# Kernel tuning notes

Hardware: AMD Instinct MI355X
Metric: run time of the kernel (lower is better)

The kernel has to match this reference:

```python
import jax, jax.numpy as jnp
import numpy as np

N = 8192          # points
M = 3             # point dimension
K_ORDER = 4       # tensor order k
C = 64            # input_in_channel
KNN = 16          # n_neighbors
NEG_SLOPE = 0.2
EPS = 1e-6


def vn_leaky_relu(v, U, neg_slope=NEG_SLOPE, eps=EPS):
    """Vector-neuron LeakyReLU. v: (n, T, C), U: (C, C) learned direction map."""
    d = jnp.einsum('ntc,cd->ntd', v, U)
    dot = jnp.sum(v * d, axis=1, keepdims=True)        # (n,1,C)
    dn2 = jnp.sum(d * d, axis=1, keepdims=True)        # (n,1,C)
    proj = (dot / (dn2 + eps)) * d
    return neg_slope * v + (1.0 - neg_slope) * jnp.where(dot >= 0, v, v - proj)


def contract_pairs(x, w, k):
    """Learned combination of all pairwise traces.
    x: (n, m,...,m (k axes), C); w: (k*(k-1)//2, C). Returns order k-2 tensor."""
    pairs = [(a, b) for a in range(1, k + 1) for b in range(a + 1, k + 1)]
    acc = None
    for i, (a, b) in enumerate(pairs):
        t = jnp.trace(x, axis1=a, axis2=b)             # (n, m^(k-2)..., C)
        acc = t * w[i] if acc is None else acc + t * w[i]
    return acc


def setup_inputs() -> dict:
    key = jax.random.key(0)
    ks = jax.random.split(key, 8)
    s1 = 1.0 / np.sqrt(C)
    s2 = 1.0 / np.sqrt(2 * C)
    return {
        'x': jax.random.normal(ks[0], (N, M), dtype=jnp.float32),
        'kron_W': jax.random.normal(ks[1], (K_ORDER, C, C), dtype=jnp.float32) * s1,
        'kron_U': jax.random.normal(ks[2], (K_ORDER, C, C), dtype=jnp.float32) * s1,
        'contr_w4': jax.random.normal(ks[3], (6, 2 * C), dtype=jnp.float32) * s2,
        'contr_W': jax.random.normal(ks[4], (2 * C, 2 * C), dtype=jnp.float32) * s2,
        'contr_U': jax.random.normal(ks[5], (2 * C, 2 * C), dtype=jnp.float32) * s2,
        'contr_w2': jax.random.normal(ks[6], (1, 2 * C), dtype=jnp.float32) * s2,
    }


def reference(x, kron_W, kron_U, contr_w4, contr_W, contr_U, contr_w2):
    n, m = x.shape
    c = kron_W.shape[-1]
    # --- brute-force kNN on x (replaces sklearn fit/kneighbors; self included,
    # static because dynamic_knn=False) ---
    sq = jnp.sum(x * x, axis=1)
    d2 = sq[:, None] + sq[None, :] - 2.0 * (x @ x.T)   # (n,n)
    _, idx = jax.lax.top_k(-d2, KNN)                   # (n,KNN) neighbor indices
    xg = x[idx]                                        # (n,KNN,m) gathered coords
    # --- Kronecker stage: v_{t+1}[i] = mean_{j in N(i)} x_j (x) v_t[j] ---
    v = jnp.ones((n, 1, c), dtype=x.dtype)
    for t in range(kron_W.shape[0]):
        vg = v[idx]                                    # (n,KNN,m^t,c)
        v = jnp.einsum('nka,nkbc->nabc', xg, vg) / KNN # (n,m,m^t,c)
        v = v.reshape(n, -1, c)                        # (n,m^(t+1),c)
        v = v @ kron_W[t]                              # CustomLinear (no bias)
        v = vn_leaky_relu(v, kron_U[t])
    # --- mean pooling + concat (pool_type=mean) ---
    g = jnp.mean(v, axis=0, keepdims=True)
    v = jnp.concatenate([v, jnp.broadcast_to(g, v.shape)], axis=2)  # (n,m^k,2c)
    c2 = 2 * c
    k = kron_W.shape[0]
    h = v.reshape((n,) + (m,) * k + (c2,))             # (n,3,3,3,3,2c)
    # --- contraction stage: k=4 -> 2 -> 0 ---
    h = contract_pairs(h, contr_w4, k)                 # (n,m,m,2c)
    h = h.reshape(n, m * m, c2) @ contr_W              # CustomLinear
    h = vn_leaky_relu(h, contr_U)
    h = h.reshape(n, m, m, c2)
    out = contract_pairs(h, contr_w2, 2)               # (n,2c)
    return out
```

## Files before the change

### kernel.cpp

```cpp
#include <hip/hip_runtime.h>
#include <math.h>

#define NPTS 8192
#define KNB  16
#define C1   64
#define C2   128
#define NEG  0.2f
#define VEPS 1e-6f
#define NCH  32
#define CHSZ (NPTS/NCH)

__device__ __forceinline__ unsigned long long expand10(unsigned v) {
    unsigned long long r = v & 0x3FFu;
    r = (r | (r << 16)) & 0x030000FFULL;
    r = (r | (r <<  8)) & 0x0300F00FULL;
    r = (r | (r <<  4)) & 0x030C30C3ULL;
    r = (r | (r <<  2)) & 0x09249249ULL;
    return r;
}

__global__ __launch_bounds__(256) void keys_kernel(const float* __restrict__ x,
                                                   unsigned long long* __restrict__ keys)
{
    const int i = blockIdx.x * 256 + threadIdx.x;
    auto cell = [](float v) -> unsigned {
        float t = (v + 6.f) * (1024.f / 12.f);
        int c = (int)t;
        c = c < 0 ? 0 : (c > 1023 ? 1023 : c);
        return (unsigned)c;
    };
    const unsigned long long m = expand10(cell(x[3*i+0]))
                               | (expand10(cell(x[3*i+1])) << 1)
                               | (expand10(cell(x[3*i+2])) << 2);
    keys[i] = (m << 13) | (unsigned long long)i;
}

__global__ __launch_bounds__(256) void rank_zero(int* __restrict__ rk)
{
    rk[blockIdx.x * 256 + threadIdx.x] = 0;
}

__global__ __launch_bounds__(256) void rank_part(const unsigned long long* __restrict__ keys,
                                                 int* __restrict__ rk)
{
    __shared__ unsigned long long sk[1024];
    const int slice = blockIdx.x & 7;
    const int qg    = blockIdx.x >> 3;
    for (int j = threadIdx.x; j < 1024; j += 256) sk[j] = keys[slice*1024 + j];
    __syncthreads();
    const int i = qg*256 + threadIdx.x;
    const unsigned long long mine = keys[i];
    int r = 0;
    for (int j = 0; j < 1024; j += 4)
        r += (int)(sk[j] < mine) + (int)(sk[j+1] < mine)
           + (int)(sk[j+2] < mine) + (int)(sk[j+3] < mine);
    atomicAdd(&rk[i], r);
}

__global__ __launch_bounds__(256) void rank_scatter(const int* __restrict__ rk,
                                                    const float* __restrict__ x,
                                                    float* __restrict__ xp,
                                                    int* __restrict__ perm)
{
    const int i = blockIdx.x * 256 + threadIdx.x;
    const int r = rk[i];
    perm[r] = i;
    xp[3*r+0] = x[3*i+0]; xp[3*r+1] = x[3*i+1]; xp[3*r+2] = x[3*i+2];
}

__global__ __launch_bounds__(256) void seedthr_kernel(const float* __restrict__ xp,
                                                      float* __restrict__ gthr)
{
    const int q = blockIdx.x * 256 + threadIdx.x;
    const float qx = xp[3*q+0], qy = xp[3*q+1], qz = xp[3*q+2];
    int lo = q - 7; lo = lo < 0 ? 0 : (lo > NPTS-16 ? NPTS-16 : lo);
    float mx = 0.f;
#pragma unroll
    for (int s = 0; s < 16; ++s) {
        const float dx = qx - xp[3*(lo+s)+0];
        const float dy = qy - xp[3*(lo+s)+1];
        const float dz = qz - xp[3*(lo+s)+2];
        mx = fmaxf(mx, fmaf(dx, dx, fmaf(dy, dy, dz*dz)));
    }
    gthr[q] = mx * 1.0002f;
}

__global__ __launch_bounds__(256) void aabb_kernel(const float* __restrict__ xp,
                                                   float* __restrict__ gaabb)
{
    __shared__ float wred[4][6];
    const int chunk = blockIdx.x;
    const int tid = threadIdx.x;
    const int j = chunk * CHSZ + tid;
    float mnx = xp[3*j+0], mny = xp[3*j+1], mnz = xp[3*j+2];
    float mxx = mnx, mxy = mny, mxz = mnz;
    for (int off = 32; off > 0; off >>= 1) {
        mnx = fminf(mnx, __shfl_down(mnx, off));
        mny = fminf(mny, __shfl_down(mny, off));
        mnz = fminf(mnz, __shfl_down(mnz, off));
        mxx = fmaxf(mxx, __shfl_down(mxx, off));
        mxy = fmaxf(mxy, __shfl_down(mxy, off));
        mxz = fmaxf(mxz, __shfl_down(mxz, off));
    }
    if ((tid & 63) == 0) {
        const int w = tid >> 6;
        wred[w][0]=mnx; wred[w][1]=mny; wred[w][2]=mnz;
        wred[w][3]=mxx; wred[w][4]=mxy; wred[w][5]=mxz;
    }
    __syncthreads();
    if (tid == 0) {
        float a0=wred[0][0], a1=wred[0][1], a2=wred[0][2];
        float a3=wred[0][3], a4=wred[0][4], a5=wred[0][5];
        for (int w = 1; w < 4; ++w) {
            a0=fminf(a0,wred[w][0]); a1=fminf(a1,wred[w][1]); a2=fminf(a2,wred[w][2]);
            a3=fmaxf(a3,wred[w][3]); a4=fmaxf(a4,wred[w][4]); a5=fmaxf(a5,wred[w][5]);
        }
        gaabb[chunk*8+0]=a0; gaabb[chunk*8+1]=a1; gaabb[chunk*8+2]=a2;
        gaabb[chunk*8+3]=a3; gaabb[chunk*8+4]=a4; gaabb[chunk*8+5]=a5;
    }
}

__global__ __launch_bounds__(256) void knn_part(const float* __restrict__ x,
                                                const float* __restrict__ gthr,
                                                const float* __restrict__ gaabb,
                                                unsigned long long* __restrict__ parts)
{
    __shared__ __align__(16) float4 cpt[4 * CHSZ];
    __shared__ unsigned long long sbuf[256 * 9];

    const int tid   = threadIdx.x;
    const int wv    = tid >> 6;
    const int lane  = tid & 63;
    const int chunk = blockIdx.x & (NCH - 1);
    const int qg    = blockIdx.x >> 5;
    const int j0    = chunk * CHSZ;
    const int q     = qg * 256 + tid;

    const float qx = x[3*q+0], qy = x[3*q+1], qz = x[3*q+2];
    float thrF = gthr[q];

    {
        const float dx = fmaxf(0.f, fmaxf(gaabb[chunk*8+0] - qx, qx - gaabb[chunk*8+3]));
        const float dy = fmaxf(0.f, fmaxf(gaabb[chunk*8+1] - qy, qy - gaabb[chunk*8+4]));
        const float dz = fmaxf(0.f, fmaxf(gaabb[chunk*8+2] - qz, qz - gaabb[chunk*8+5]));
        const float lb = fmaf(dx, dx, fmaf(dy, dy, dz*dz)) * 0.9998f;
        if (__all(lb > thrF)) {
#pragma unroll
            for (int r = 0; r < 16; ++r)
                parts[((size_t)chunk * KNB + r) * NPTS + q] = ~0ull;
            return;
        }
    }

    float4* wcpt = cpt + wv * CHSZ;
#pragma unroll
    for (int s = 0; s < 4; ++s) {
        const int j = lane + 64*s;
        wcpt[j] = make_float4(x[3*(j0+j)+0], x[3*(j0+j)+1], x[3*(j0+j)+2], 0.f);
    }

    unsigned long long bd[16];
#pragma unroll
    for (int r = 0; r < 16; ++r) bd[r] = ~0ull;
    int cnt = 0;
    unsigned long long* mybuf = sbuf + tid * 9;

    auto flush = [&]() {
#pragma unroll
        for (int s = 0; s < 8; ++s) {
            if (s < cnt) {
                const unsigned long long k = mybuf[s];
                if (k < bd[15]) {
#pragma unroll
                    for (int p2 = 15; p2 > 0; --p2) {
                        const bool sh = k < bd[p2-1];
                        const bool pl = k < bd[p2];
                        bd[p2] = sh ? bd[p2-1] : (pl ? k : bd[p2]);
                    }
                    if (k < bd[0]) bd[0] = k;
                }
            }
        }
        cnt = 0;
        if (bd[15] != ~0ull) {
            const double dub = __longlong_as_double((long long)(bd[15] | 8191ull));
            thrF = fminf(thrF, (float)dub * 1.0001f);
        }
    };

    for (int jj = 0; jj < CHSZ; jj += 4) {
        const float4 p0 = wcpt[jj+0];
        const float4 p1 = wcpt[jj+1];
        const float4 p2 = wcpt[jj+2];
        const float4 p3 = wcpt[jj+3];
#pragma unroll
        for (int u = 0; u < 4; ++u) {
            const float4 p = (u==0) ? p0 : (u==1) ? p1 : (u==2) ? p2 : p3;
            const float dx = qx - p.x, dy = qy - p.y, dz = qz - p.z;
            const float d2f = fmaf(dx, dx, fmaf(dy, dy, dz*dz));
            if (d2f <= thrF) {
                const double ddx = (double)dx, ddy = (double)dy, ddz = (double)dz;
                const double d2 = ddx*ddx + ddy*ddy + ddz*ddz;
                const unsigned long long key =
                    (((unsigned long long)__double_as_longlong(d2)) & ~8191ull)
                    | (unsigned long long)(j0 + jj + u);
                if (key < bd[15]) { mybuf[cnt] = key; ++cnt; }
            }
        }
        if (__any(cnt >= 5)) flush();
    }
    flush();

#pragma unroll
    for (int r = 0; r < 16; ++r)
        parts[((size_t)chunk * KNB + r) * NPTS + q] = bd[r];
}

__global__ __launch_bounds__(256) void knn_merge(const unsigned long long* __restrict__ parts,
                                                 int* __restrict__ idx_out)
{
    __shared__ unsigned char heads[256][NCH];
    const int tid = threadIdx.x;
    const int q = blockIdx.x * 256 + tid;
    unsigned char* h = heads[tid];
#pragma unroll
    for (int c = 0; c < NCH; ++c) h[c] = 0;
    for (int r = 0; r < KNB; ++r) {
        unsigned long long best = ~0ull; int bc = 0;
#pragma unroll
        for (int c = 0; c < NCH; ++c) {
            const unsigned long long k = parts[((size_t)c * KNB + h[c]) * NPTS + q];
            if (k < best) { best = k; bc = c; }
        }
        h[bc]++;
        idx_out[q*KNB + r] = (int)(best & 8191ull);
    }
}

__global__ __launch_bounds__(256) void prep_kernel(const float* __restrict__ kW,
                                                   const float* __restrict__ kU,
                                                   float* __restrict__ scol,
                                                   float* __restrict__ bcat)
{
    __shared__ float sW[64*64];
    __shared__ float sS[64];
    const int t = blockIdx.x;
    const int tid = threadIdx.x;
    if (t == 0) {
        for (int e = tid; e < 64*64; e += 256) sW[e] = kW[e];
        __syncthreads();
        if (tid < 64) {
            float s = 0.f;
            for (int j = 0; j < 64; ++j) s += sW[j*64 + tid];
            sS[tid] = s;
        }
        __syncthreads();
        if (tid < 64) {
            float s2 = 0.f;
            for (int j = 0; j < 64; ++j) s2 = fmaf(sS[j], kU[j*64 + tid], s2);
            scol[tid]      = sS[tid];
            scol[64 + tid] = s2;
        }
    } else {
        const float* W = kW + t*4096;
        const float* U = kU + t*4096;
        for (int e = tid; e < 64*64; e += 256) sW[e] = W[e];
        __syncthreads();
        float* B = bcat + (size_t)(t-1)*64*128;
        for (int o = tid; o < 64*64; o += 256) {
            const int j = o >> 6, c = o & 63;
            float s = 0.f;
            for (int l = 0; l < 64; ++l) s = fmaf(sW[j*64 + l], U[l*64 + c], s);
            B[j*128 + c]      = sW[j*64 + c];
            B[j*128 + 64 + c] = s;
        }
    }
}

__global__ __launch_bounds__(256) void step1_kernel(const float* __restrict__ xp,
                                                    const int* __restrict__ idxs,
                                                    const float* __restrict__ scol,
                                                    float* __restrict__ R1)
{
    const int pt = blockIdx.x * 256 + threadIdx.x;
    float mx0 = 0.f, mx1 = 0.f, mx2 = 0.f;
#pragma unroll
    for (int k = 0; k < KNB; ++k) {
        const int id = idxs[pt*KNB + k];
        mx0 += xp[3*id+0]; mx1 += xp[3*id+1]; mx2 += xp[3*id+2];
    }
    const float inv = 1.0f / KNB;
    mx0 *= inv; mx1 *= inv; mx2 *= inv;
    const float S2 = mx0*mx0 + mx1*mx1 + mx2*mx2;
    float* op = R1 + (size_t)pt * 192;
    for (int c = 0; c < 64; ++c) {
        const float sc = scol[c], su = scol[64 + c];
        const float dt = S2 * sc * su;
        const float dn = S2 * su * su;
        const float m  = (dt < 0.f) ? 0.8f * dt / (dn + VEPS) : 0.f;
        const float rc = fmaf(-m, su, sc);
        op[c]       = mx0 * rc;
        op[64 + c]  = mx1 * rc;
        op[128 + c] = mx2 * rc;
    }
}

#define FMA4(ar, b0, b1, b2, b3, acc) \
    acc.x = fmaf(ar.x,b0.x, fmaf(ar.y,b1.x, fmaf(ar.z,b2.x, fmaf(ar.w,b3.x, acc.x)))); \
    acc.y = fmaf(ar.x,b0.y, fmaf(ar.y,b1.y, fmaf(ar.z,b2.y, fmaf(ar.w,b3.y, acc.y)))); \
    acc.z = fmaf(ar.x,b0.z, fmaf(ar.y,b1.z, fmaf(ar.z,b2.z, fmaf(ar.w,b3.z, acc.z)))); \
    acc.w = fmaf(ar.x,b0.w, fmaf(ar.y,b1.w, fmaf(ar.z,b2.w, fmaf(ar.w,b3.w, acc.w))));

__global__ __launch_bounds__(256) void zgemm_kernel(const float* __restrict__ R,
                                                    const float* __restrict__ Bcat,
                                                    float* __restrict__ YwZ)
{
    constexpr int SA = 68;
    __shared__ __align__(16) float sA[64*SA];
    __shared__ __align__(16) float sB[64*128];
    const int tid = threadIdx.x;
    const size_t row0 = (size_t)blockIdx.x * 64;

    for (int e4 = tid; e4 < 1024; e4 += 256) {
        const int r = e4 >> 4, c4 = (e4 & 15) * 4;
        *reinterpret_cast<float4*>(sA + r*SA + c4) =
            *reinterpret_cast<const float4*>(R + (row0 + r)*64 + c4);
    }
    for (int e4 = tid; e4 < 2048; e4 += 256) {
        const int j = e4 >> 5, c4 = (e4 & 31) * 4;
        *reinterpret_cast<float4*>(sB + j*128 + c4) =
            *reinterpret_cast<const float4*>(Bcat + j*128 + c4);
    }
    __syncthreads();

    const int rg = tid >> 5;
    const int d  = (tid & 31) * 4;
    float4 acc0={0,0,0,0},acc1=acc0,acc2=acc0,acc3=acc0,acc4=acc0,acc5=acc0,acc6=acc0,acc7=acc0;
    for (int c = 0; c < 64; c += 4) {
        const float4 b0 = *reinterpret_cast<const float4*>(sB + (c+0)*128 + d);
        const float4 b1 = *reinterpret_cast<const float4*>(sB + (c+1)*128 + d);
        const float4 b2 = *reinterpret_cast<const float4*>(sB + (c+2)*128 + d);
        const float4 b3 = *reinterpret_cast<const float4*>(sB + (c+3)*128 + d);
        float4 a;
        a = *reinterpret_cast<const float4*>(sA + (rg*8+0)*SA + c); FMA4(a,b0,b1,b2,b3,acc0);
        a = *reinterpret_cast<const float4*>(sA + (rg*8+1)*SA + c); FMA4(a,b0,b1,b2,b3,acc1);
        a = *reinterpret_cast<const float4*>(sA + (rg*8+2)*SA + c); FMA4(a,b0,b1,b2,b3,acc2);
        a = *reinterpret_cast<const float4*>(sA + (rg*8+3)*SA + c); FMA4(a,b0,b1,b2,b3,acc3);
        a = *reinterpret_cast<const float4*>(sA + (rg*8+4)*SA + c); FMA4(a,b0,b1,b2,b3,acc4);
        a = *reinterpret_cast<const float4*>(sA + (rg*8+5)*SA + c); FMA4(a,b0,b1,b2,b3,acc5);
        a = *reinterpret_cast<const float4*>(sA + (rg*8+6)*SA + c); FMA4(a,b0,b1,b2,b3,acc6);
        a = *reinterpret_cast<const float4*>(sA + (rg*8+7)*SA + c); FMA4(a,b0,b1,b2,b3,acc7);
    }
    float* op = YwZ + (row0 + rg*8)*128 + d;
    *reinterpret_cast<float4*>(op + 0*128) = acc0;
    *reinterpret_cast<float4*>(op + 1*128) = acc1;
    *reinterpret_cast<float4*>(op + 2*128) = acc2;
    *reinterpret_cast<float4*>(op + 3*128) = acc3;
    *reinterpret_cast<float4*>(op + 4*128) = acc4;
    *reinterpret_cast<float4*>(op + 5*128) = acc5;
    *reinterpret_cast<float4*>(op + 6*128) = acc6;
    *reinterpret_cast<float4*>(op + 7*128) = acc7;
}

template<int PINP, int TT>
__global__ __launch_bounds__(256) void gather_kernel(
    const float* __restrict__ xp, const int* __restrict__ idxs,
    const float* __restrict__ yz,
    float* __restrict__ Rout,
    int ppb)
{
    constexpr int PCW = PINP * 128;
    constexpr int NSL = PCW / 4;
    constexpr int TC  = TT * 64;

    __shared__ __align__(16) float buf[TT * 128];
    __shared__ int   sIds[KNB];
    __shared__ float sXg[KNB*3];
    __shared__ float pdt[4][64], pdn[4][64], msc[64];

    const int tid   = threadIdx.x;
    const int slots = gridDim.x >> 3;
    const int xcd   = blockIdx.x & 7;
    const int slot  = blockIdx.x >> 3;
    const int base  = xcd * slots * ppb;

    for (int pi = 0; pi < ppb; ++pi) {
        const int pt = base + pi * slots + slot;
        if (tid < KNB) {
            const int id = idxs[pt*KNB + tid];
            sIds[tid] = id;
            sXg[tid*3+0] = xp[3*id+0];
            sXg[tid*3+1] = xp[3*id+1];
            sXg[tid*3+2] = xp[3*id+2];
        }
        __syncthreads();

        float xr[KNB*3];
#pragma unroll
        for (int e = 0; e < KNB*3; ++e) xr[e] = sXg[e];

        for (int sl = tid; sl < NSL; sl += 256) {
            const int b  = sl >> 5;
            const int cc = (sl & 31) * 4;
            float4 s0 = {0,0,0,0}, s1 = s0, s2 = s0;
#pragma unroll
            for (int k = 0; k < KNB; ++k) {
                const float4 val = *reinterpret_cast<const float4*>(
                    yz + (size_t)sIds[k]*PCW + b*128 + cc);
                const float xa = xr[k*3+0], xb = xr[k*3+1], xc = xr[k*3+2];
                s0.x=fmaf(xa,val.x,s0.x); s0.y=fmaf(xa,val.y,s0.y);
                s0.z=fmaf(xa,val.z,s0.z); s0.w=fmaf(xa,val.w,s0.w);
                s1.x=fmaf(xb,val.x,s1.x); s1.y=fmaf(xb,val.y,s1.y);
                s1.z=fmaf(xb,val.z,s1.z); s1.w=fmaf(xb,val.w,s1.w);
                s2.x=fmaf(xc,val.x,s2.x); s2.y=fmaf(xc,val.y,s2.y);
                s2.z=fmaf(xc,val.z,s2.z); s2.w=fmaf(xc,val.w,s2.w);
            }
            const float inv = 1.0f / KNB;
            s0.x*=inv; s0.y*=inv; s0.z*=inv; s0.w*=inv;
            s1.x*=inv; s1.y*=inv; s1.z*=inv; s1.w*=inv;
            s2.x*=inv; s2.y*=inv; s2.z*=inv; s2.w*=inv;
            *reinterpret_cast<float4*>(buf + (0*PINP + b)*128 + cc) = s0;
            *reinterpret_cast<float4*>(buf + (1*PINP + b)*128 + cc) = s1;
            *reinterpret_cast<float4*>(buf + (2*PINP + b)*128 + cc) = s2;
        }
        __syncthreads();
        {
            const int c = tid & 63, g = tid >> 6;
            float dt = 0.f, dn = 0.f;
            for (int t = g; t < TT; t += 4) {
                const float vv = buf[t*128 + c], dd = buf[t*128 + 64 + c];
                dt = fmaf(vv, dd, dt); dn = fmaf(dd, dd, dn);
            }
            pdt[g][c] = dt; pdn[g][c] = dn;
        }
        __syncthreads();
        if (tid < 64) {
            const float dt = pdt[0][tid]+pdt[1][tid]+pdt[2][tid]+pdt[3][tid];
            const float dn = pdn[0][tid]+pdn[1][tid]+pdn[2][tid]+pdn[3][tid];
            msc[tid] = (dt < 0.f) ? 0.8f * dt / (dn + VEPS) : 0.f;
        }
        __syncthreads();
        {
            float* op = Rout + (size_t)pt * TC;
            for (int e = tid; e < TC; e += 256) {
                const int t = e >> 6, c = e & 63;
                op[e] = fmaf(-msc[c], buf[t*128 + 64 + c], buf[t*128 + c]);
            }
        }
        __syncthreads();
    }
}

#define FMAQS(acc, s, val) \
    acc.x = fmaf(s, val.x, acc.x); acc.y = fmaf(s, val.y, acc.y); \
    acc.z = fmaf(s, val.z, acc.z); acc.w = fmaf(s, val.w, acc.w);

__global__ __launch_bounds__(256) void gather4_kernel(
    const float* __restrict__ xp, const int* __restrict__ idxs,
    const float* __restrict__ yz,
    const float* __restrict__ w4,
    float* __restrict__ hv, float* __restrict__ gpart,
    int ppb)
{
    constexpr int TT = 81;
    constexpr int CH = 32;
    constexpr int SB = 68;
    constexpr int NG = (TT*CH + 255) / 256;

    __shared__ __align__(16) float buf[TT * SB];
    __shared__ int   sIds[KNB];
    __shared__ float sXg[KNB*3];
    __shared__ float pdt[27][33], pdn[27][33];
    __shared__ float msc[CH];

    const int tid   = threadIdx.x;
    const int xcd   = blockIdx.x & 7;
    const int r2    = blockIdx.x >> 3;
    const int half  = r2 & 1;
    const int slot  = r2 >> 1;
    const int slots = gridDim.x >> 4;
    const int base0 = xcd * slots * ppb;
    const int c0    = half * CH;
    const int eff   = xcd * slots + slot;

    const int ub  = tid >> 3;
    const int ucq = tid & 7;
    const bool act = (ub < 27);
    const int srcV = ub*128 + c0 + ucq*4;
    const int srcD = srcV + 64;

    float gacc[NG];
#pragma unroll
    for (int i = 0; i < NG; ++i) gacc[i] = 0.f;

    for (int pi = 0; pi < ppb; ++pi) {
        const int pt = base0 + pi * slots + slot;
        if (tid < KNB) {
            const int id = idxs[pt*KNB + tid];
            sIds[tid] = id;
            sXg[tid*3+0] = xp[3*id+0];
            sXg[tid*3+1] = xp[3*id+1];
            sXg[tid*3+2] = xp[3*id+2];
        }
        __syncthreads();

        if (act) {
            float4 vA[3], dA[3];
#pragma unroll
            for (int a = 0; a < 3; ++a) { vA[a] = make_float4(0,0,0,0); dA[a] = vA[a]; }
#pragma unroll
            for (int k = 0; k < KNB; ++k) {
                const float* rowp = yz + (size_t)sIds[k]*3456;
                const float4 vq = *reinterpret_cast<const float4*>(rowp + srcV);
                const float4 dq = *reinterpret_cast<const float4*>(rowp + srcD);
                const float xa = sXg[k*3+0], xb = sXg[k*3+1], xc = sXg[k*3+2];
                FMAQS(vA[0], xa, vq) FMAQS(vA[1], xb, vq) FMAQS(vA[2], xc, vq)
                FMAQS(dA[0], xa, dq) FMAQS(dA[1], xb, dq) FMAQS(dA[2], xc, dq)
            }
            const float inv = 1.0f / KNB;
            float4 dt4 = make_float4(0,0,0,0), dn4 = dt4;
#pragma unroll
            for (int a = 0; a < 3; ++a) {
                vA[a].x*=inv; vA[a].y*=inv; vA[a].z*=inv; vA[a].w*=inv;
                dA[a].x*=inv; dA[a].y*=inv; dA[a].z*=inv; dA[a].w*=inv;
                dt4.x = fmaf(vA[a].x, dA[a].x, dt4.x);
                dt4.y = fmaf(vA[a].y, dA[a].y, dt4.y);
                dt4.z = fmaf(vA[a].z, dA[a].z, dt4.z);
                dt4.w = fmaf(vA[a].w, dA[a].w, dt4.w);
                dn4.x = fmaf(dA[a].x, dA[a].x, dn4.x);
                dn4.y = fmaf(dA[a].y, dA[a].y, dn4.y);
                dn4.z = fmaf(dA[a].z, dA[a].z, dn4.z);
                dn4.w = fmaf(dA[a].w, dA[a].w, dn4.w);
                float* bp = buf + (a*27 + ub)*SB;
                *reinterpret_cast<float4*>(bp + ucq*4)      = vA[a];
                *reinterpret_cast<float4*>(bp + 32 + ucq*4) = dA[a];
            }
            pdt[ub][ucq*4+0] = dt4.x; pdt[ub][ucq*4+1] = dt4.y;
            pdt[ub][ucq*4+2] = dt4.z; pdt[ub][ucq*4+3] = dt4.w;
            pdn[ub][ucq*4+0] = dn4.x; pdn[ub][ucq*4+1] = dn4.y;
            pdn[ub][ucq*4+2] = dn4.z; pdn[ub][ucq*4+3] = dn4.w;
        }
        __syncthreads();
        if (tid < CH) {
            float dt = 0.f, dn = 0.f;
#pragma unroll
            for (int b2 = 0; b2 < 27; ++b2) { dt += pdt[b2][tid]; dn += pdn[b2][tid]; }
            msc[tid] = (dt < 0.f) ? 0.8f * dt / (dn + VEPS) : 0.f;
        }
        __syncthreads();
#pragma unroll
        for (int i = 0; i < NG; ++i) {
            const int e = i*256 + tid;
            if (e < TT*CH) {
                const int t = e >> 5, cc = e & 31;
                const float v = fmaf(-msc[cc], buf[t*SB + 32 + cc], buf[t*SB + cc]);
                buf[t*SB + cc] = v;
                gacc[i] += v;
            }
        }
        __syncthreads();
        for (int e = tid; e < 9*CH; e += 256) {
            const int pq = e >> 5, cc = e & 31;
            const int p = pq / 3, qq = pq - 3*p;
            const int c = c0 + cc;
            float tr0=0,tr1=0,tr2=0,tr3=0,tr4=0,tr5=0;
#pragma unroll
            for (int r = 0; r < 3; ++r) {
                tr0 += buf[(r*36 + p*3 + qq )*SB + cc];
                tr1 += buf[(r*30 + p*9 + qq )*SB + cc];
                tr2 += buf[(r*28 + p*9 + qq*3)*SB + cc];
                tr3 += buf[(p*27 + r*12 + qq )*SB + cc];
                tr4 += buf[(p*27 + r*10 + qq*3)*SB + cc];
                tr5 += buf[(p*27 + qq*9 + r*4 )*SB + cc];
            }
            hv[(size_t)pt*576 + pq*64 + c] =
                  w4[0*C2 + c]*tr0 + w4[1*C2 + c]*tr1 + w4[2*C2 + c]*tr2
                + w4[3*C2 + c]*tr3 + w4[4*C2 + c]*tr4 + w4[5*C2 + c]*tr5;
        }
        __syncthreads();
    }
    float* gp = gpart + (size_t)eff * 5184;
#pragma unroll
    for (int i = 0; i < NG; ++i) {
        const int e = i*256 + tid;
        if (e < TT*CH) {
            const int t = e >> 5, cc = e & 31;
            gp[t*64 + c0 + cc] = gacc[i];
        }
    }
}

__global__ __launch_bounds__(256) void reduce_g_kernel(const float* __restrict__ gpart,
                                                       float* __restrict__ g)
{
    __shared__ float red[256];
    const int el = threadIdx.x & 15, pg = threadIdx.x >> 4;
    const int e = blockIdx.x * 16 + el;
    float s = 0.f;
    for (int p = pg; p < 2048; p += 16) s += gpart[(size_t)p * (81*C1) + e];
    red[threadIdx.x] = s;
    __syncthreads();
    for (int st = 8; st > 0; st >>= 1) {
        if (pg < st) red[el + 16*pg] += red[el + 16*(pg+st)];
        __syncthreads();
    }
    if (pg == 0) g[e] = red[el] * (1.0f/NPTS);
}

__global__ __launch_bounds__(256) void hgw_kernel(const float* __restrict__ g,
                                                  const float* __restrict__ w4,
                                                  const float* __restrict__ cW,
                                                  float* __restrict__ hgW)
{
    __shared__ float gs[81*C1];
    __shared__ float hg[9*C1];
    const int tid = threadIdx.x;
    for (int e = tid; e < 81*C1; e += 256) gs[e] = g[e];
    __syncthreads();
    for (int e = tid; e < 9*C1; e += 256) {
        const int pq = e >> 6, c = e & 63;
        const int p = pq / 3, qq = pq - 3*p;
        float tr0=0,tr1=0,tr2=0,tr3=0,tr4=0,tr5=0;
#pragma unroll
        for (int r = 0; r < 3; ++r) {
            tr0 += gs[(r*36 + p*3 + qq ) * C1 + c];
            tr1 += gs[(r*30 + p*9 + qq ) * C1 + c];
            tr2 += gs[(r*28 + p*9 + qq*3) * C1 + c];
            tr3 += gs[(p*27 + r*12 + qq ) * C1 + c];
            tr4 += gs[(p*27 + r*10 + qq*3) * C1 + c];
            tr5 += gs[(p*27 + qq*9 + r*4 ) * C1 + c];
        }
        hg[e] = w4[0*C2 + 64 + c]*tr0 + w4[1*C2 + 64 + c]*tr1 + w4[2*C2 + 64 + c]*tr2
              + w4[3*C2 + 64 + c]*tr3 + w4[4*C2 + 64 + c]*tr4 + w4[5*C2 + 64 + c]*tr5;
    }
    __syncthreads();
    for (int o = tid; o < 9*C2; o += 256) {
        const int t = o >> 7, c = o & 127;
        float s = 0.f;
        for (int j = 0; j < C1; ++j) s = fmaf(hg[t*C1 + j], cW[(C1+j)*C2 + c], s);
        hgW[o] = s;
    }
}

__global__ __launch_bounds__(256) void contract_kernel(const float* __restrict__ hv,
                                                       const float* __restrict__ hgW,
                                                       const float* __restrict__ cW,
                                                       const float* __restrict__ cU,
                                                       const float* __restrict__ w2,
                                                       const int* __restrict__ perm,
                                                       float* __restrict__ out,
                                                       int ppb)
{
    constexpr int S0 = C1 + 4;
    constexpr int SH = C2 + 4;
    __shared__ __align__(16) float h0[36*S0];
    __shared__ __align__(16) float h1[36*SH];
    __shared__ __align__(16) float h2[36*SH];
    __shared__ __align__(16) float hgs[9*C2];
    __shared__ int sPerm[4];

    const int tid = threadIdx.x;
    for (int e = tid; e < 9*C2; e += 256) hgs[e] = hgW[e];
    __syncthreads();

    const int iters = ppb >> 2;
    for (int it = 0; it < iters; ++it) {
        const int base = blockIdx.x * ppb + it * 4;
        if (tid < 4) sPerm[tid] = perm[base + tid];
        for (int e = tid; e < 4*9*C1; e += 256) {
            const int pt = e / 576, rem = e - pt*576;
            const int t = rem >> 6, c = rem & 63;
            h0[(pt*9 + t)*S0 + c] = hv[(size_t)(base+pt)*576 + rem];
        }
        __syncthreads();
        for (int u = tid; u < 9*32; u += 256) {
            const int tg = u >> 5;
            const int d  = (u & 31) * 4;
            const int r0 = tg*4;
            float4 acc0 = *reinterpret_cast<const float4*>(hgs + ((r0+0)%9)*C2 + d);
            float4 acc1 = *reinterpret_cast<const float4*>(hgs + ((r0+1)%9)*C2 + d);
            float4 acc2 = *reinterpret_cast<const float4*>(hgs + ((r0+2)%9)*C2 + d);
            float4 acc3 = *reinterpret_cast<const float4*>(hgs + ((r0+3)%9)*C2 + d);
            for (int c = 0; c < C1; c += 4) {
                const float4 a0 = *reinterpret_cast<const float4*>(h0 + (r0+0)*S0 + c);
                const float4 a1 = *reinterpret_cast<const float4*>(h0 + (r0+1)*S0 + c);
                const float4 a2 = *reinterpret_cast<const float4*>(h0 + (r0+2)*S0 + c);
                const float4 a3 = *reinterpret_cast<const float4*>(h0 + (r0+3)*S0 + c);
                const float4 b0 = *reinterpret_cast<const float4*>(cW + (c+0)*C2 + d);
                const float4 b1 = *reinterpret_cast<const float4*>(cW + (c+1)*C2 + d);
                const float4 b2 = *reinterpret_cast<const float4*>(cW + (c+2)*C2 + d);
                const float4 b3 = *reinterpret_cast<const float4*>(cW + (c+3)*C2 + d);
                FMA4(a0, b0, b1, b2, b3, acc0);
                FMA4(a1, b0, b1, b2, b3, acc1);
                FMA4(a2, b0, b1, b2, b3, acc2);
                FMA4(a3, b0, b1, b2, b3, acc3);
            }
            *reinterpret_cast<float4*>(h1 + (r0+0)*SH + d) = acc0;
            *reinterpret_cast<float4*>(h1 + (r0+1)*SH + d) = acc1;
            *reinterpret_cast<float4*>(h1 + (r0+2)*SH + d) = acc2;
            *reinterpret_cast<float4*>(h1 + (r0+3)*SH + d) = acc3;
        }
        __syncthreads();
        for (int u = tid; u < 9*32; u += 256) {
            const int tg = u >> 5;
            const int d  = (u & 31) * 4;
            const int r0 = tg*4;
            float4 acc0 = {0,0,0,0}, acc1 = acc0, acc2 = acc0, acc3 = acc0;
            for (int c = 0; c < C2; c += 4) {
                const float4 a0 = *reinterpret_cast<const float4*>(h1 + (r0+0)*SH + c);
                const float4 a1 = *reinterpret_cast<const float4*>(h1 + (r0+1)*SH + c);
                const float4 a2 = *reinterpret_cast<const float4*>(h1 + (r0+2)*SH + c);
                const float4 a3 = *reinterpret_cast<const float4*>(h1 + (r0+3)*SH + c);
                const float4 b0 = *reinterpret_cast<const float4*>(cU + (c+0)*C2 + d);
                const float4 b1 = *reinterpret_cast<const float4*>(cU + (c+1)*C2 + d);
                const float4 b2 = *reinterpret_cast<const float4*>(cU + (c+2)*C2 + d);
                const float4 b3 = *reinterpret_cast<const float4*>(cU + (c+3)*C2 + d);
                FMA4(a0, b0, b1, b2, b3, acc0);
                FMA4(a1, b0, b1, b2, b3, acc1);
                FMA4(a2, b0, b1, b2, b3, acc2);
                FMA4(a3, b0, b1, b2, b3, acc3);
            }
            *reinterpret_cast<float4*>(h2 + (r0+0)*SH + d) = acc0;
            *reinterpret_cast<float4*>(h2 + (r0+1)*SH + d) = acc1;
            *reinterpret_cast<float4*>(h2 + (r0+2)*SH + d) = acc2;
            *reinterpret_cast<float4*>(h2 + (r0+3)*SH + d) = acc3;
        }
        __syncthreads();
#pragma unroll
        for (int p2 = 0; p2 < 2; ++p2) {
            const int pair = tid + 256*p2;
            const int pt = pair >> 7, c = pair & 127;
            float dt = 0.f, dn = 0.f;
            for (int t = 0; t < 9; ++t) {
                const float vv = h1[(pt*9+t)*SH + c], dd = h2[(pt*9+t)*SH + c];
                dt = fmaf(vv, dd, dt); dn = fmaf(dd, dd, dn);
            }
            const float m = (dt < 0.f) ? 0.8f * dt / (dn + VEPS) : 0.f;
            float s = 0.f;
#pragma unroll
            for (int r = 0; r < 3; ++r) {
                const int t = r * 4;
                s += fmaf(-m, h2[(pt*9+t)*SH + c], h1[(pt*9+t)*SH + c]);
            }
            out[(size_t)sPerm[pt]*C2 + c] = w2[c] * s;
        }
        __syncthreads();
    }
}

extern "C" void kernel_launch(void* const* d_in, const int* in_sizes, int n_in,
                              void* d_out, int out_size, void* d_ws, size_t ws_size,
                              hipStream_t stream)
{
    (void)in_sizes; (void)n_in; (void)out_size; (void)ws_size;
    const float* x  = (const float*)d_in[0];
    const float* kW = (const float*)d_in[1];
    const float* kU = (const float*)d_in[2];
    const float* w4 = (const float*)d_in[3];
    const float* cW = (const float*)d_in[4];
    const float* cU = (const float*)d_in[5];
    const float* w2 = (const float*)d_in[6];
    float* out = (float*)d_out;

    char* ws = (char*)d_ws;
    size_t off = 0;
    auto alloc = [&](size_t bytes) -> void* {
        void* p = ws + off; off += (bytes + 255) & ~(size_t)255; return p;
    };
    int*   idx   = (int*)  alloc((size_t)NPTS*KNB*4);
    float* xp    = (float*)alloc((size_t)NPTS*3*4);
    unsigned long long* keys = (unsigned long long*)alloc((size_t)NPTS*8);
    int*   perm  = (int*)  alloc((size_t)NPTS*4);
    int*   rk    = (int*)  alloc((size_t)NPTS*4);
    float* gthr  = (float*)alloc((size_t)NPTS*4);
    float* gaabb = (float*)alloc((size_t)NCH*8*4);
    float* scol  = (float*)alloc(128*4);
    float* bcat  = (float*)alloc((size_t)3*64*128*4);
    float* R1    = (float*)alloc((size_t)NPTS*3*C1*4);
    float* YwZ2  = (float*)alloc((size_t)NPTS*3*C2*4);
    float* R2    = (float*)alloc((size_t)NPTS*9*C1*4);
    float* YwZ3  = (float*)alloc((size_t)NPTS*9*C2*4);
    float* R3    = (float*)alloc((size_t)NPTS*27*C1*4);
    float* YwZ4  = (float*)alloc((size_t)NPTS*27*C2*4);
    float* g     = (float*)alloc((size_t)81*C1*4);
    float* hgW   = (float*)alloc((size_t)9*C2*4);

    float* hv    = R1;
    float* gpart = R2;
    unsigned long long* parts = (unsigned long long*)YwZ4;

    keys_kernel <<<NPTS/256, 256, 0, stream>>>(x, keys);
    rank_zero   <<<NPTS/256, 256, 0, stream>>>(rk);
    rank_part   <<<256, 256, 0, stream>>>(keys, rk);
    rank_scatter<<<NPTS/256, 256, 0, stream>>>(rk, x, xp, perm);
    seedthr_kernel<<<NPTS/256, 256, 0, stream>>>(xp, gthr);
    aabb_kernel <<<NCH, 256, 0, stream>>>(xp, gaabb);
    knn_part    <<<32*NCH, 256, 0, stream>>>(xp, gthr, gaabb, parts);
    knn_merge   <<<NPTS/256, 256, 0, stream>>>(parts, idx);
    prep_kernel <<<4, 256, 0, stream>>>(kW, kU, scol, bcat);
    step1_kernel<<<NPTS/256, 256, 0, stream>>>(xp, idx, scol, R1);

    zgemm_kernel<<<NPTS*3/64,  256, 0, stream>>>(R1, bcat,            YwZ2);
    gather_kernel<3, 9>  <<<2048, 256, 0, stream>>>(xp, idx, YwZ2, R2, 4);
    zgemm_kernel<<<NPTS*9/64,  256, 0, stream>>>(R2, bcat + 8192,     YwZ3);
    gather_kernel<9, 27> <<<2048, 256, 0, stream>>>(xp, idx, YwZ3, R3, 4);
    zgemm_kernel<<<NPTS*27/64, 256, 0, stream>>>(R3, bcat + 16384,    YwZ4);
    gather4_kernel<<<4096, 256, 0, stream>>>(xp, idx, YwZ4, w4, hv, gpart, 4);

    reduce_g_kernel<<<324, 256, 0, stream>>>(gpart, g);
    hgw_kernel<<<1, 256, 0, stream>>>(g, w4, cW, hgW);
    contract_kernel<<<1024, 256, 0, stream>>>(hv, hgW, cW, cU, w2, perm, out, 8);
}
```

Measured before the change: 693.4 us.

## Fuse chunked kNN search and merge into a single per-query kernel

Result: slower. 1.106 ms (+59.5%).

```diff
diff --git a/kernel.cpp b/kernel.cpp
--- a/kernel.cpp
+++ b/kernel.cpp
@@ -120,50 +120,24 @@
     }
 }
 
-__global__ __launch_bounds__(256) void knn_part(const float* __restrict__ x,
-                                                const float* __restrict__ gthr,
-                                                const float* __restrict__ gaabb,
-                                                unsigned long long* __restrict__ parts)
-{
-    __shared__ __align__(16) float4 cpt[4 * CHSZ];
-    __shared__ unsigned long long sbuf[256 * 9];
-
-    const int tid   = threadIdx.x;
-    const int wv    = tid >> 6;
-    const int lane  = tid & 63;
-    const int chunk = blockIdx.x & (NCH - 1);
-    const int qg    = blockIdx.x >> 5;
-    const int j0    = chunk * CHSZ;
-    const int q     = qg * 256 + tid;
-
-    const float qx = x[3*q+0], qy = x[3*q+1], qz = x[3*q+2];
+__global__ __launch_bounds__(64) void knn_direct(const float* __restrict__ xp,
+                                                 const float* __restrict__ gthr,
+                                                 const float* __restrict__ gaabb,
+                                                 int* __restrict__ idx_out)
+{
+    __shared__ __align__(16) float4 cpt[CHSZ];
+    __shared__ unsigned long long sbuf[64 * 9];
+
+    const int lane = threadIdx.x;
+    const int q    = blockIdx.x * 64 + lane;
+    const float qx = xp[3*q+0], qy = xp[3*q+1], qz = xp[3*q+2];
     float thrF = gthr[q];
-
-    {
-        const float dx = fmaxf(0.f, fmaxf(gaabb[chunk*8+0] - qx, qx - gaabb[chunk*8+3]));
-        const float dy = fmaxf(0.f, fmaxf(gaabb[chunk*8+1] - qy, qy - gaabb[chunk*8+4]));
-        const float dz = fmaxf(0.f, fmaxf(gaabb[chunk*8+2] - qz, qz - gaabb[chunk*8+5]));
-        const float lb = fmaf(dx, dx, fmaf(dy, dy, dz*dz)) * 0.9998f;
-        if (__all(lb > thrF)) {
-#pragma unroll
-            for (int r = 0; r < 16; ++r)
-                parts[((size_t)chunk * KNB + r) * NPTS + q] = ~0ull;
-            return;
-        }
-    }
-
-    float4* wcpt = cpt + wv * CHSZ;
-#pragma unroll
-    for (int s = 0; s < 4; ++s) {
-        const int j = lane + 64*s;
-        wcpt[j] = make_float4(x[3*(j0+j)+0], x[3*(j0+j)+1], x[3*(j0+j)+2], 0.f);
-    }
 
     unsigned long long bd[16];
 #pragma unroll
     for (int r = 0; r < 16; ++r) bd[r] = ~0ull;
     int cnt = 0;
-    unsigned long long* mybuf = sbuf + tid * 9;
+    unsigned long long* mybuf = sbuf + lane * 9;
 
     auto flush = [&]() {
 #pragma unroll
@@ -188,53 +162,52 @@
         }
     };
 
-    for (int jj = 0; jj < CHSZ; jj += 4) {
-        const float4 p0 = wcpt[jj+0];
-        const float4 p1 = wcpt[jj+1];
-        const float4 p2 = wcpt[jj+2];
-        const float4 p3 = wcpt[jj+3];
-#pragma unroll
-        for (int u = 0; u < 4; ++u) {
-            const float4 p = (u==0) ? p0 : (u==1) ? p1 : (u==2) ? p2 : p3;
-            const float dx = qx - p.x, dy = qy - p.y, dz = qz - p.z;
-            const float d2f = fmaf(dx, dx, fmaf(dy, dy, dz*dz));
-            if (d2f <= thrF) {
-                const double ddx = (double)dx, ddy = (double)dy, ddz = (double)dz;
-                const double d2 = ddx*ddx + ddy*ddy + ddz*ddz;
-                const unsigned long long key =
-                    (((unsigned long long)__double_as_longlong(d2)) & ~8191ull)
-                    | (unsigned long long)(j0 + jj + u);
-                if (key < bd[15]) { mybuf[cnt] = key; ++cnt; }
-            }
-        }
-        if (__any(cnt >= 5)) flush();
-    }
-    flush();
+    const int own = (blockIdx.x * 64) / CHSZ;
+    for (int cc = 0; cc < NCH; ++cc) {
+        const int chunk = (own + cc) & (NCH - 1);
+        {
+            const float dx = fmaxf(0.f, fmaxf(gaabb[chunk*8+0] - qx, qx - gaabb[chunk*8+3]));
+            const float dy = fmaxf(0.f, fmaxf(gaabb[chunk*8+1] - qy, qy - gaabb[chunk*8+4]));
+            const float dz = fmaxf(0.f, fmaxf(gaabb[chunk*8+2] - qz, qz - gaabb[chunk*8+5]));
+            const float lb = fmaf(dx, dx, fmaf(dy, dy, dz*dz)) * 0.9998f;
+            if (__all(lb > thrF)) continue;
+        }
+        const int j0 = chunk * CHSZ;
+        __syncthreads();
+#pragma unroll
+        for (int s = 0; s < 4; ++s) {
+            const int j = lane + 64*s;
+            cpt[j] = make_float4(xp[3*(j0+j)+0], xp[3*(j0+j)+1], xp[3*(j0+j)+2], 0.f);
+        }
+        __syncthreads();
+
+        for (int jj = 0; jj < CHSZ; jj += 4) {
+            const float4 p0 = cpt[jj+0];
+            const float4 p1 = cpt[jj+1];
+            const float4 p2 = cpt[jj+2];
+            const float4 p3 = cpt[jj+3];
+#pragma unroll
+            for (int u = 0; u < 4; ++u) {
+                const float4 p = (u==0) ? p0 : (u==1) ? p1 : (u==2) ? p2 : p3;
+                const float dx = qx - p.x, dy = qy - p.y, dz = qz - p.z;
+                const float d2f = fmaf(dx, dx, fmaf(dy, dy, dz*dz));
+                if (d2f <= thrF) {
+                    const double ddx = (double)dx, ddy = (double)dy, ddz = (double)dz;
+                    const double d2 = ddx*ddx + ddy*ddy + ddz*ddz;
+                    const unsigned long long key =
+                        (((unsigned long long)__double_as_longlong(d2)) & ~8191ull)
+                        | (unsigned long long)(j0 + jj + u);
+                    if (key < bd[15]) { mybuf[cnt] = key; ++cnt; }
+                }
+            }
+            if (__any(cnt >= 5)) flush();
+        }
+        flush();
+    }
 
 #pragma unroll
     for (int r = 0; r < 16; ++r)
-        parts[((size_t)chunk * KNB + r) * NPTS + q] = bd[r];
-}
-
-__global__ __launch_bounds__(256) void knn_merge(const unsigned long long* __restrict__ parts,
-                                                 int* __restrict__ idx_out)
-{
-    __shared__ unsigned char heads[256][NCH];
-    const int tid = threadIdx.x;
-    const int q = blockIdx.x * 256 + tid;
-    unsigned char* h = heads[tid];
-#pragma unroll
-    for (int c = 0; c < NCH; ++c) h[c] = 0;
-    for (int r = 0; r < KNB; ++r) {
-        unsigned long long best = ~0ull; int bc = 0;
-#pragma unroll
-        for (int c = 0; c < NCH; ++c) {
-            const unsigned long long k = parts[((size_t)c * KNB + h[c]) * NPTS + q];
-            if (k < best) { best = k; bc = c; }
-        }
-        h[bc]++;
-        idx_out[q*KNB + r] = (int)(best & 8191ull);
-    }
+        idx_out[q*KNB + r] = (int)(bd[r] & 8191ull);
 }
 
 __global__ __launch_bounds__(256) void prep_kernel(const float* __restrict__ kW,
@@ -787,7 +760,6 @@
 
     float* hv    = R1;
     float* gpart = R2;
-    unsigned long long* parts = (unsigned long long*)YwZ4;
 
     keys_kernel <<<NPTS/256, 256, 0, stream>>>(x, keys);
     rank_zero   <<<NPTS/256, 256, 0, stream>>>(rk);
@@ -795,8 +767,7 @@
     rank_scatter<<<NPTS/256, 256, 0, stream>>>(rk, x, xp, perm);
     seedthr_kernel<<<NPTS/256, 256, 0, stream>>>(xp, gthr);
     aabb_kernel <<<NCH, 256, 0, stream>>>(xp, gaabb);
-    knn_part    <<<32*NCH, 256, 0, stream>>>(xp, gthr, gaabb, parts);
-    knn_merge   <<<NPTS/256, 256, 0, stream>>>(parts, idx);
+    knn_direct  <<<NPTS/64, 64, 0, stream>>>(xp, gthr, gaabb, idx);
     prep_kernel <<<4, 256, 0, stream>>>(kW, kU, scol, bcat);
     step1_kernel<<<NPTS/256, 256, 0, stream>>>(xp, idx, scol, R1);
 
```
